# Kernel tuning notes

Measured on AMD Instinct MI355X. Metric: run time of the kernel, lower is better.

The kernel has to match this reference:

```python
import jax, jax.numpy as jnp
import numpy as np

BN_EPS = 1e-5


def conv1x1(x, w, b):
    # x: [B, C, H, W], w: [O, C], b: [O]
    return jnp.einsum('bchw,oc->bohw', x, w) + b[None, :, None, None]


def cca(x, wq, bq, wk, bk, wv, bv, wg, bg):
    # Criss-cross attention block: full HWxHW attention with qk dim = C//8
    B, C, H, W = x.shape
    N = H * W
    q = conv1x1(x, wq, bq).reshape(B, -1, N)   # [B, C//8, N]
    k = conv1x1(x, wk, bk).reshape(B, -1, N)   # [B, C//8, N]
    v = conv1x1(x, wv, bv).reshape(B, C, N)    # [B, C, N]
    att = jax.nn.softmax(jnp.einsum('bdq,bdk->bqk', q, k), axis=-1)  # [B, N, N]
    out = jnp.einsum('bck,bqk->bcq', v, att).reshape(B, C, H, W)
    return x + conv1x1(out, wg, bg)


def setup_inputs() -> dict:
    key = jax.random.key(0)
    ks = iter(jax.random.split(key, 64))

    def rn(shape, s=0.1):
        return jax.random.normal(next(ks), shape, dtype=jnp.float32) * s

    C_IN = [48, 96, 192, 384]
    OC = 8            # hardcoded out_channels in the module
    NOUT = 19         # num_outputs
    LC = OC * 4       # last_inp_channels
    d = {}
    d['x0'] = rn((2, 48, 96, 96), 1.0)
    d['x1'] = rn((2, 96, 48, 48), 1.0)
    d['x2'] = rn((2, 192, 24, 24), 1.0)
    d['x3'] = rn((2, 384, 12, 12), 1.0)
    for i, c in enumerate(C_IN):
        d[f'w{i}'] = rn((OC, c))
        d[f'b{i}'] = rn((OC,))
    # cca3 params are never used by the original forward (it calls cca1 on x_3),
    # so only cca0/cca1/cca2 are materialized.
    for i in range(3):
        d[f'cca{i}_wq'] = rn((OC // 8, OC)); d[f'cca{i}_bq'] = rn((OC // 8,))
        d[f'cca{i}_wk'] = rn((OC // 8, OC)); d[f'cca{i}_bk'] = rn((OC // 8,))
        d[f'cca{i}_wv'] = rn((OC, OC));      d[f'cca{i}_bv'] = rn((OC,))
        d[f'cca{i}_wg'] = rn((OC, OC));      d[f'cca{i}_bg'] = rn((OC,))
    d['wl0'] = rn((LC, LC)); d['bl0'] = rn((LC,))
    d['bn_s'] = jnp.ones((LC,), jnp.float32)
    d['bn_b'] = jnp.zeros((LC,), jnp.float32)
    d['bn_m'] = rn((LC,), 0.01)
    d['bn_v'] = jnp.ones((LC,), jnp.float32)
    d['wl1'] = rn((NOUT, LC)); d['bl1'] = rn((NOUT,))
    return d


def reference(x0, x1, x2, x3, w0, b0, w1, b1, w2, b2, w3, b3,
              cca0_wq, cca0_bq, cca0_wk, cca0_bk, cca0_wv, cca0_bv, cca0_wg, cca0_bg,
              cca1_wq, cca1_bq, cca1_wk, cca1_bk, cca1_wv, cca1_bv, cca1_wg, cca1_bg,
              cca2_wq, cca2_bq, cca2_wk, cca2_bk, cca2_wv, cca2_bv, cca2_wg, cca2_bg,
              wl0, bl0, bn_s, bn_b, bn_m, bn_v, wl1, bl1):
    y0 = cca(conv1x1(x0, w0, b0), cca0_wq, cca0_bq, cca0_wk, cca0_bk, cca0_wv, cca0_bv, cca0_wg, cca0_bg)
    y1 = cca(conv1x1(x1, w1, b1), cca1_wq, cca1_bq, cca1_wk, cca1_bk, cca1_wv, cca1_bv, cca1_wg, cca1_bg)
    y2 = cca(conv1x1(x2, w2, b2), cca2_wq, cca2_bq, cca2_wk, cca2_bk, cca2_wv, cca2_bv, cca2_wg, cca2_bg)
    # NOTE: original torch code applies cca1 (not cca3) to x_3 -- reproduced faithfully.
    y3 = cca(conv1x1(x3, w3, b3), cca1_wq, cca1_bq, cca1_wk, cca1_bk, cca1_wv, cca1_bv, cca1_wg, cca1_bg)

    B, C, H0, W0 = y0.shape

    def up(t):
        # torch F.interpolate(mode='bilinear', align_corners=False) == jax half-pixel bilinear
        return jax.image.resize(t, (t.shape[0], t.shape[1], H0, W0), method='bilinear')

    x = jnp.concatenate([y0, up(y1), up(y2), up(y3)], axis=1)  # [B, 32, H0, W0]
    x = conv1x1(x, wl0, bl0)
    scale = (bn_s / jnp.sqrt(bn_v + BN_EPS))[None, :, None, None]
    x = (x - bn_m[None, :, None, None]) * scale + bn_b[None, :, None, None]
    x = jax.nn.relu(x)
    return conv1x1(x, wl1, bl1)
```

## Files before the change

### kernel.cpp

```cpp
#include <hip/hip_runtime.h>
#include <math.h>

#define LB __launch_bounds__(256)

#define NSLOT 24480
#define MT 28
#define NMOM 252

typedef float f32x4 __attribute__((ext_vector_type(4)));

struct QkvmArgs {
  const float *x0, *x1, *x2, *x3;
  const float *w0, *w1, *w2, *w3;
  const float *c0, *c1, *c2, *c3;
  const float *wq[4], *bq[4], *wk[4], *bk[4], *wv[4], *bv[4];
  float *P, *Q;
  unsigned long long *MOM;
};

template<int CG>
__device__ __forceinline__ void qkvm_body(const QkvmArgs& a, const int scale, const int C,
    const int N, const int slotoff, const int rel,
    const float* __restrict__ xp, const float* __restrict__ wp, const float* __restrict__ bp,
    float* s_w, float* s_sm, float* s_red, float* s_kp, float* s_v) {
  constexpr int PX = 256 / CG;
  const int tid = threadIdx.x;
  for (int i = tid; i < 8*C; i += 256) { const int c = i >> 3, o = i & 7; s_w[i] = wp[o*C + c]; }
  if (tid >= 128 && tid < 192) { const int t = tid - 128; s_sm[32 + t] = a.wv[scale][(t & 7)*8 + (t >> 3)]; }
  if (tid < 8) {
    s_sm[tid]      = bp[tid];
    s_sm[8 + tid]  = a.wq[scale][tid];
    s_sm[16 + tid] = a.wk[scale][tid];
    s_sm[24 + tid] = a.bv[scale][tid];
  }
  if (tid == 96) { s_sm[96] = a.bq[scale][0]; s_sm[97] = a.bk[scale][0]; }
  __syncthreads();

  const int bpb = N / PX;
  const int b = rel / bpb, blk = rel - b*bpb;
  const int px = tid & (PX - 1), cg = tid / PX;
  const int n = blk*PX + px;
  const float* xb = xp + (size_t)b*C*N + n;
  float p[8];
  #pragma unroll
  for (int o = 0; o < 8; ++o) p[o] = 0.f;
  const int c0 = cg*12;
  #pragma unroll
  for (int cc = 0; cc < 12; cc += 4) {
    const int c = c0 + cc;
    const float xv0 = xb[(size_t)(c+0)*N];
    const float xv1 = xb[(size_t)(c+1)*N];
    const float xv2 = xb[(size_t)(c+2)*N];
    const float xv3 = xb[(size_t)(c+3)*N];
    #pragma unroll
    for (int o = 0; o < 8; ++o) p[o] = fmaf(s_w[(c+0)*8+o], xv0, p[o]);
    #pragma unroll
    for (int o = 0; o < 8; ++o) p[o] = fmaf(s_w[(c+1)*8+o], xv1, p[o]);
    #pragma unroll
    for (int o = 0; o < 8; ++o) p[o] = fmaf(s_w[(c+2)*8+o], xv2, p[o]);
    #pragma unroll
    for (int o = 0; o < 8; ++o) p[o] = fmaf(s_w[(c+3)*8+o], xv3, p[o]);
  }
  f32x4* sp = (f32x4*)&s_red[tid*8];
  sp[0] = (f32x4){p[0], p[1], p[2], p[3]};
  sp[1] = (f32x4){p[4], p[5], p[6], p[7]};
  __syncthreads();

  if (tid < PX) {
    float pc[8];
    #pragma unroll
    for (int o = 0; o < 8; ++o) {
      float s = s_sm[o];
      #pragma unroll
      for (int g = 0; g < CG; ++g) s += s_red[(g*PX + tid)*8 + o];
      pc[o] = s;
    }
    float q = s_sm[96], kv = s_sm[97];
    #pragma unroll
    for (int c = 0; c < 8; ++c) { q = fmaf(s_sm[8+c], pc[c], q); kv = fmaf(s_sm[16+c], pc[c], kv); }
    float v[8];
    #pragma unroll
    for (int o = 0; o < 8; ++o) v[o] = s_sm[24 + o];
    #pragma unroll
    for (int c = 0; c < 8; ++c) {
      const float pcc = pc[c];
      #pragma unroll
      for (int o = 0; o < 8; ++o) v[o] = fmaf(s_sm[32 + c*8 + o], pcc, v[o]);
    }
    const int g = slotoff + b*N + n;
    f32x4* Pp = (f32x4*)&a.P[(size_t)g*8];
    Pp[0] = (f32x4){pc[0], pc[1], pc[2], pc[3]};
    Pp[1] = (f32x4){pc[4], pc[5], pc[6], pc[7]};
    a.Q[g] = q;
    s_kp[tid*MT] = 1.f;
    float pw = 1.f;
    #pragma unroll
    for (int m = 1; m < MT; ++m) { pw *= kv; s_kp[tid*MT + m] = pw; }
    #pragma unroll
    for (int j = 0; j < 8; ++j) s_v[tid*8 + j] = v[j];
  }
  __syncthreads();

  if (tid < NMOM) {
    const int m = tid / 9, j = tid - m*9;
    float acc = 0.f;
    if (j == 0) {
      #pragma unroll 8
      for (int e = 0; e < PX; ++e) acc += s_kp[e*MT + m];
    } else {
      #pragma unroll 8
      for (int e = 0; e < PX; ++e) acc = fmaf(s_kp[e*MT + m], s_v[e*8 + (j-1)], acc);
    }
    const long long iq = llrintf(ldexpf(acc, 30 - m));
    atomicAdd(&a.MOM[(size_t)(scale*2 + b)*NMOM + tid], (unsigned long long)iq);
  }
}

__global__ LB void qkvm_kernel(QkvmArgs a) {
  __shared__ __align__(16) float s_w[3072];
  __shared__ __align__(16) float s_sm[104];
  __shared__ __align__(16) float s_red[256*8];
  __shared__ __align__(16) float s_kp[64*MT];
  __shared__ __align__(16) float s_v[64*8];
  const int bid = blockIdx.x;
  if (bid < 288)      qkvm_body<4> (a, 0, 48,  9216, 0,     bid,     a.x0, a.w0, a.c0, s_w, s_sm, s_red, s_kp, s_v);
  else if (bid < 432) qkvm_body<8> (a, 1, 96,  2304, 18432, bid-288, a.x1, a.w1, a.c1, s_w, s_sm, s_red, s_kp, s_v);
  else if (bid < 504) qkvm_body<16>(a, 2, 192, 576,  23040, bid-432, a.x2, a.w2, a.c2, s_w, s_sm, s_red, s_kp, s_v);
  else                qkvm_body<32>(a, 3, 384, 144,  24192, bid-504, a.x3, a.w3, a.c3, s_w, s_sm, s_red, s_kp, s_v);
}

struct FinArgs {
  const float *Q, *P;
  const unsigned long long *MOM;
  const float *wg0, *bg0, *wg1, *bg1, *wg2, *bg2;
  float *Y;
};

__global__ LB void finish_kernel(FinArgs a) {
  __shared__ __align__(16) float smom[8*MT*12];
  __shared__ float swg[3][64], sbg[3][8];
  const int tid = threadIdx.x;
  for (int i = tid; i < 8*MT*12; i += 256) smom[i] = 0.f;
  if (tid < 64) { swg[0][tid] = a.wg0[tid]; swg[1][tid] = a.wg1[tid]; swg[2][tid] = a.wg2[tid]; }
  if (tid < 8)  { sbg[0][tid] = a.bg0[tid]; sbg[1][tid] = a.bg1[tid]; sbg[2][tid] = a.bg2[tid]; }
  __syncthreads();
  for (int i = tid; i < 8*NMOM; i += 256) {
    const int sbi = i / NMOM, r = i - sbi*NMOM;
    const int m = r / 9, j = r - m*9;
    const long long ll = (long long)a.MOM[i];
    smom[sbi*(MT*12) + m*12 + j] = (float)ll * exp2f((float)(m - 30));
  }
  __syncthreads();
  const int g = blockIdx.x*256 + tid;
  if (g >= NSLOT) return;
  int scale, N, off, widx;
  if (g < 18432)      { scale=0; N=9216; off=0;     widx=0; }
  else if (g < 23040) { scale=1; N=2304; off=18432; widx=1; }
  else if (g < 24192) { scale=2; N=576;  off=23040; widx=2; }
  else                { scale=3; N=144;  off=24192; widx=1; }
  const int b = (g - off >= N) ? 1 : 0;
  const int sb = scale*2 + b;
  const float q = a.Q[g];
  const float* mb = &smom[sb*(MT*12)];
  float t = 1.f, den = 0.f;
  float num[8];
  #pragma unroll
  for (int c = 0; c < 8; ++c) num[c] = 0.f;
  #pragma unroll
  for (int m = 0; m < MT; ++m) {
    const f32x4 a0 = *(const f32x4*)&mb[m*12];
    const f32x4 a1 = *(const f32x4*)&mb[m*12 + 4];
    const f32x4 a2 = *(const f32x4*)&mb[m*12 + 8];
    den    = fmaf(t, a0.x, den);
    num[0] = fmaf(t, a0.y, num[0]); num[1] = fmaf(t, a0.z, num[1]); num[2] = fmaf(t, a0.w, num[2]);
    num[3] = fmaf(t, a1.x, num[3]); num[4] = fmaf(t, a1.y, num[4]); num[5] = fmaf(t, a1.z, num[5]);
    num[6] = fmaf(t, a1.w, num[6]); num[7] = fmaf(t, a2.x, num[7]);
    if (m + 1 < MT) t *= q * (1.f/(float)(m+1));
  }
  const float inv = 1.f/den;
  float o8[8];
  #pragma unroll
  for (int c = 0; c < 8; ++c) o8[c] = num[c]*inv;
  const f32x4 pA = *(const f32x4*)&a.P[(size_t)g*8];
  const f32x4 pB = *(const f32x4*)&a.P[(size_t)g*8 + 4];
  const float pv[8] = {pA.x, pA.y, pA.z, pA.w, pB.x, pB.y, pB.z, pB.w};
  const float* wg = swg[widx];
  float y[8];
  #pragma unroll
  for (int o = 0; o < 8; ++o) {
    float s2 = pv[o] + sbg[widx][o];
    #pragma unroll
    for (int c = 0; c < 8; ++c) s2 = fmaf(wg[o*8 + c], o8[c], s2);
    y[o] = s2;
  }
  f32x4* Yp = (f32x4*)&a.Y[(size_t)g*8];
  Yp[0] = (f32x4){y[0], y[1], y[2], y[3]};
  Yp[1] = (f32x4){y[4], y[5], y[6], y[7]};
}

template<int HS>
__device__ inline void bilerp8(float* zo, const float* Yb, int h, int w) {
  constexpr float inv = (float)HS/96.0f;
  const float sy = (h + 0.5f)*inv - 0.5f;
  const float sx = (w + 0.5f)*inv - 0.5f;
  const int iy0 = (int)floorf(sy); const float fy = sy - (float)iy0;
  const int ix0 = (int)floorf(sx); const float fx = sx - (float)ix0;
  const int y0 = min(max(iy0, 0), HS-1), y1 = min(max(iy0 + 1, 0), HS-1);
  const int x0 = min(max(ix0, 0), HS-1), x1 = min(max(ix0 + 1, 0), HS-1);
  const float* p00 = &Yb[(size_t)(y0*HS + x0)*8];
  const float* p01 = &Yb[(size_t)(y0*HS + x1)*8];
  const float* p10 = &Yb[(size_t)(y1*HS + x0)*8];
  const float* p11 = &Yb[(size_t)(y1*HS + x1)*8];
  const float w00 = (1.f-fy)*(1.f-fx), w01 = (1.f-fy)*fx, w10 = fy*(1.f-fx), w11 = fy*fx;
  #pragma unroll
  for (int c = 0; c < 8; ++c)
    zo[c] = w00*p00[c] + w01*p01[c] + w10*p10[c] + w11*p11[c];
}

__global__ LB void head_kernel(const float* __restrict__ Y,
                               const float* wl0, const float* bl0,
                               const float* bn_s, const float* bn_b,
                               const float* bn_m, const float* bn_v,
                               const float* wl1, const float* bl1,
                               float* __restrict__ out) {
  __shared__ float s_wl0[1024], s_wl1[608];
  __shared__ float s_bl0[32], s_sc[32], s_sh[32], s_bl1[19];
  const int tid = threadIdx.x;
  for (int i = tid; i < 1024; i += 256) s_wl0[i] = wl0[i];
  for (int i = tid; i < 608;  i += 256) s_wl1[i] = wl1[i];
  if (tid < 32) {
    s_bl0[tid] = bl0[tid];
    const float sc = bn_s[tid] / sqrtf(bn_v[tid] + 1e-5f);
    s_sc[tid] = sc;
    s_sh[tid] = bn_b[tid] - bn_m[tid]*sc;
  }
  if (tid >= 32 && tid < 51) s_bl1[tid - 32] = bl1[tid - 32];
  __syncthreads();
  const int gp = blockIdx.x*256 + tid;
  const int b = (gp >= 9216) ? 1 : 0;
  const int n = gp - b*9216;
  const int h = n / 96, w = n - h*96;
  float z[32];
  {
    const float4 zA = *(const float4*)&Y[(size_t)(b*9216 + n)*8];
    const float4 zB = *(const float4*)&Y[(size_t)(b*9216 + n)*8 + 4];
    z[0]=zA.x; z[1]=zA.y; z[2]=zA.z; z[3]=zA.w; z[4]=zB.x; z[5]=zB.y; z[6]=zB.z; z[7]=zB.w;
  }
  bilerp8<48>(z + 8,  &Y[(size_t)(18432 + b*2304)*8], h, w);
  bilerp8<24>(z + 16, &Y[(size_t)(23040 + b*576)*8],  h, w);
  bilerp8<12>(z + 24, &Y[(size_t)(24192 + b*144)*8],  h, w);
  float o19[19];
  #pragma unroll
  for (int j = 0; j < 19; ++j) o19[j] = s_bl1[j];
  #pragma unroll 1
  for (int o = 0; o < 32; ++o) {
    float sA = s_bl0[o], sB = 0.f;
    #pragma unroll
    for (int c4 = 0; c4 < 4; ++c4) {
      const float4 wv = *(const float4*)&s_wl0[o*32 + c4*4];
      sA = fmaf(wv.x, z[c4*4+0], sA);
      sA = fmaf(wv.y, z[c4*4+1], sA);
      sA = fmaf(wv.z, z[c4*4+2], sA);
      sA = fmaf(wv.w, z[c4*4+3], sA);
    }
    #pragma unroll
    for (int c4 = 4; c4 < 8; ++c4) {
      const float4 wv = *(const float4*)&s_wl0[o*32 + c4*4];
      sB = fmaf(wv.x, z[c4*4+0], sB);
      sB = fmaf(wv.y, z[c4*4+1], sB);
      sB = fmaf(wv.z, z[c4*4+2], sB);
      sB = fmaf(wv.w, z[c4*4+3], sB);
    }
    const float t = fmaxf(fmaf(sA + sB, s_sc[o], s_sh[o]), 0.f);
    #pragma unroll
    for (int j = 0; j < 19; ++j) o19[j] = fmaf(s_wl1[j*32 + o], t, o19[j]);
  }
  #pragma unroll
  for (int j = 0; j < 19; ++j)
    out[((size_t)b*19 + j)*9216 + n] = o19[j];
}

extern "C" void kernel_launch(void* const* d_in, const int* in_sizes, int n_in,
                              void* d_out, int out_size, void* d_ws, size_t ws_size,
                              hipStream_t stream) {
  (void)in_sizes; (void)n_in; (void)out_size; (void)ws_size;
  const float* wq[3]; const float* bq[3]; const float* wk[3]; const float* bk[3];
  const float* wv[3]; const float* bv[3]; const float* wg[3]; const float* bg[3];
  for (int i = 0; i < 3; ++i) {
    const int base = 12 + i*8;
    wq[i] = (const float*)d_in[base + 0]; bq[i] = (const float*)d_in[base + 1];
    wk[i] = (const float*)d_in[base + 2]; bk[i] = (const float*)d_in[base + 3];
    wv[i] = (const float*)d_in[base + 4]; bv[i] = (const float*)d_in[base + 5];
    wg[i] = (const float*)d_in[base + 6]; bg[i] = (const float*)d_in[base + 7];
  }
  const int m4[4] = {0, 1, 2, 1};

  float* ws = (float*)d_ws;
  float* P = ws;
  float* Q = P + (size_t)NSLOT*8;
  unsigned long long* MOM = (unsigned long long*)(Q + NSLOT);
  float* Y = (float*)(MOM + 8*NMOM);

  QkvmArgs qa;
  qa.x0 = (const float*)d_in[0]; qa.x1 = (const float*)d_in[1];
  qa.x2 = (const float*)d_in[2]; qa.x3 = (const float*)d_in[3];
  qa.w0 = (const float*)d_in[4];  qa.c0 = (const float*)d_in[5];
  qa.w1 = (const float*)d_in[6];  qa.c1 = (const float*)d_in[7];
  qa.w2 = (const float*)d_in[8];  qa.c2 = (const float*)d_in[9];
  qa.w3 = (const float*)d_in[10]; qa.c3 = (const float*)d_in[11];
  for (int s = 0; s < 4; ++s) {
    qa.wq[s] = wq[m4[s]]; qa.bq[s] = bq[m4[s]];
    qa.wk[s] = wk[m4[s]]; qa.bk[s] = bk[m4[s]];
    qa.wv[s] = wv[m4[s]]; qa.bv[s] = bv[m4[s]];
  }
  qa.P = P; qa.Q = Q; qa.MOM = MOM;

  FinArgs fa;
  fa.Q = Q; fa.P = P; fa.MOM = MOM;
  fa.wg0 = wg[0]; fa.bg0 = bg[0];
  fa.wg1 = wg[1]; fa.bg1 = bg[1];
  fa.wg2 = wg[2]; fa.bg2 = bg[2];
  fa.Y = Y;

  hipMemsetAsync(MOM, 0, (size_t)8*NMOM*sizeof(unsigned long long), stream);
  qkvm_kernel<<<540, 256, 0, stream>>>(qa);
  finish_kernel<<<96, 256, 0, stream>>>(fa);
  head_kernel<<<72, 256, 0, stream>>>(Y, (const float*)d_in[36], (const float*)d_in[37],
                                      (const float*)d_in[38], (const float*)d_in[39],
                                      (const float*)d_in[40], (const float*)d_in[41],
                                      (const float*)d_in[42], (const float*)d_in[43],
                                      (float*)d_out);
}
```

Before: 35.28 us.

## Replace fixed-point atomic moment accumulation with per-block partials reduced in finish

Each qkvm block now writes its float moment partials to a per-block buffer instead of quantizing them to fixed point and atomically adding into a shared accumulator. The finish kernel reduces the partials for each scale/batch slot. This drops the memset launch and the contention on the 64-bit atomics. In exchange, each of the 96 finish blocks redundantly re-reads up to 144 partials per moment, which adds global load traffic.

```diff
diff --git a/kernel.cpp b/kernel.cpp
--- a/kernel.cpp
+++ b/kernel.cpp
@@ -6,6 +6,7 @@
 #define NSLOT 24480
 #define MT 28
 #define NMOM 252
+#define NBLK_Q 540
 
 typedef float f32x4 __attribute__((ext_vector_type(4)));
 
@@ -15,7 +16,7 @@
   const float *c0, *c1, *c2, *c3;
   const float *wq[4], *bq[4], *wk[4], *bk[4], *wv[4], *bv[4];
   float *P, *Q;
-  unsigned long long *MOM;
+  float *MOMP;
 };
 
 template<int CG>
@@ -111,8 +112,7 @@
       #pragma unroll 8
       for (int e = 0; e < PX; ++e) acc = fmaf(s_kp[e*MT + m], s_v[e*8 + (j-1)], acc);
     }
-    const long long iq = llrintf(ldexpf(acc, 30 - m));
-    atomicAdd(&a.MOM[(size_t)(scale*2 + b)*NMOM + tid], (unsigned long long)iq);
+    a.MOMP[(size_t)blockIdx.x*NMOM + tid] = acc;
   }
 }
 
@@ -130,8 +130,7 @@
 }
 
 struct FinArgs {
-  const float *Q, *P;
-  const unsigned long long *MOM;
+  const float *Q, *P, *MOMP;
   const float *wg0, *bg0, *wg1, *bg1, *wg2, *bg2;
   float *Y;
 };
@@ -144,11 +143,17 @@
   if (tid < 64) { swg[0][tid] = a.wg0[tid]; swg[1][tid] = a.wg1[tid]; swg[2][tid] = a.wg2[tid]; }
   if (tid < 8)  { sbg[0][tid] = a.bg0[tid]; sbg[1][tid] = a.bg1[tid]; sbg[2][tid] = a.bg2[tid]; }
   __syncthreads();
+  const int start[8] = {0, 144, 288, 360, 432, 468, 504, 522};
+  const int cnt[8]   = {144, 144, 72, 72, 36, 36, 18, 18};
   for (int i = tid; i < 8*NMOM; i += 256) {
     const int sbi = i / NMOM, r = i - sbi*NMOM;
     const int m = r / 9, j = r - m*9;
-    const long long ll = (long long)a.MOM[i];
-    smom[sbi*(MT*12) + m*12 + j] = (float)ll * exp2f((float)(m - 30));
+    const float* bp2 = a.MOMP + (size_t)start[sbi]*NMOM + r;
+    float s = 0.f;
+    const int c2 = cnt[sbi];
+    #pragma unroll 4
+    for (int t2 = 0; t2 < c2; ++t2) s += bp2[(size_t)t2*NMOM];
+    smom[sbi*(MT*12) + m*12 + j] = s;
   }
   __syncthreads();
   const int g = blockIdx.x*256 + tid;
@@ -298,8 +303,8 @@
   float* ws = (float*)d_ws;
   float* P = ws;
   float* Q = P + (size_t)NSLOT*8;
-  unsigned long long* MOM = (unsigned long long*)(Q + NSLOT);
-  float* Y = (float*)(MOM + 8*NMOM);
+  float* MOMP = Q + NSLOT;
+  float* Y = MOMP + (size_t)NBLK_Q*NMOM;
 
   QkvmArgs qa;
   qa.x0 = (const float*)d_in[0]; qa.x1 = (const float*)d_in[1];
@@ -313,17 +318,16 @@
     qa.wk[s] = wk[m4[s]]; qa.bk[s] = bk[m4[s]];
     qa.wv[s] = wv[m4[s]]; qa.bv[s] = bv[m4[s]];
   }
-  qa.P = P; qa.Q = Q; qa.MOM = MOM;
+  qa.P = P; qa.Q = Q; qa.MOMP = MOMP;
 
   FinArgs fa;
-  fa.Q = Q; fa.P = P; fa.MOM = MOM;
+  fa.Q = Q; fa.P = P; fa.MOMP = MOMP;
   fa.wg0 = wg[0]; fa.bg0 = bg[0];
   fa.wg1 = wg[1]; fa.bg1 = bg[1];
   fa.wg2 = wg[2]; fa.bg2 = bg[2];
   fa.Y = Y;
 
-  hipMemsetAsync(MOM, 0, (size_t)8*NMOM*sizeof(unsigned long long), stream);
-  qkvm_kernel<<<540, 256, 0, stream>>>(qa);
+  qkvm_kernel<<<NBLK_Q, 256, 0, stream>>>(qa);
   finish_kernel<<<96, 256, 0, stream>>>(fa);
   head_kernel<<<72, 256, 0, stream>>>(Y, (const float*)d_in[36], (const float*)d_in[37],
                                       (const float*)d_in[38], (const float*)d_in[39],
```

Measured after the change: 65.83 us. +86.6%, slower.
